# Kernel optimization log

Hardware: AMD Instinct MI355X
Metric: run time of the kernel (lower is better)

## Reference

```python
import jax, jax.numpy as jnp
import numpy as np

B, MAXT, MAXU, A = 16, 200, 101, 512
BLANK = 0


def setup_inputs() -> dict:
    key = jax.random.key(0)
    k1, k2, k3, k4 = jax.random.split(key, 4)
    logits = jax.random.normal(k1, (B, MAXT, MAXU, A), dtype=jnp.float32)
    log_probs = jax.nn.log_softmax(logits, axis=-1)  # transducer expects log-softmaxed acts
    labels = jax.random.randint(k2, (B, MAXU - 1), 1, A, dtype=jnp.int32)  # non-blank targets
    T = jax.random.randint(k3, (B,), MAXT // 2, MAXT + 1, dtype=jnp.int32)  # frames per utt
    U = jax.random.randint(k4, (B,), (MAXU - 1) // 2, MAXU, dtype=jnp.int32)  # labels per utt, <= MAXU-1
    return {"log_probs": log_probs, "labels": labels, "T": T, "U": U}


def _alpha_lattice(blk, emit):
    """RNN-T forward variables.
    blk, emit: [B, T, U] log-probs of blank / correct label at each lattice cell.
    Recurrence: alpha[t,u] = logaddexp(alpha[t-1,u]+blk[t-1,u], alpha[t,u-1]+emit[t,u-1]).
    Within a time step the u-recursion is solved in closed form with a
    log-cumsum-exp (associative_scan of logaddexp), so the only sequential
    loop is the scan over t.
    """
    Bb, Tm, Um = blk.shape

    def prefix_emit(emit_t):  # c[u] = sum_{k<u} emit_t[k]
        return jnp.concatenate(
            [jnp.zeros((Bb, 1), emit_t.dtype), jnp.cumsum(emit_t[:, :-1], axis=1)], axis=1)

    alpha0 = prefix_emit(emit[:, 0])  # alpha[0,u] = sum of first u emits, alpha[0,0]=0

    def step(alpha_prev, inputs):
        blk_tm1, emit_t = inputs            # [B, U] each
        a = alpha_prev + blk_tm1            # no-emit entry point per u
        c = prefix_emit(emit_t)
        # alpha[t,u] = c[u] + LSE_{u'<=u}(a[u'] - c[u'])
        alpha_t = c + jax.lax.associative_scan(jnp.logaddexp, a - c, axis=1)
        return alpha_t, alpha_t

    xs = (jnp.moveaxis(blk[:, :-1], 1, 0), jnp.moveaxis(emit[:, 1:], 1, 0))
    _, rest = jax.lax.scan(step, alpha0, xs)          # [T-1, B, U]
    alpha = jnp.concatenate([alpha0[None], rest], axis=0)  # [T, B, U]
    return jnp.moveaxis(alpha, 0, 1)                  # [B, T, U]


def reference(log_probs, labels, T, U):
    Bb, Tm, Um, _ = log_probs.shape
    blk = log_probs[..., BLANK]                       # [B, T, U]
    lab = jnp.concatenate([labels, jnp.zeros((Bb, 1), labels.dtype)], axis=1)  # pad to [B, U]
    idx = jnp.broadcast_to(lab[:, None, :, None], (Bb, Tm, Um, 1))
    emit = jnp.take_along_axis(log_probs, idx, axis=3)[..., 0]  # log P(label_u | t, u)
    alpha = _alpha_lattice(blk, emit)
    bidx = jnp.arange(Bb)
    # log_p = alpha[T-1, U] + blank emission at terminal cell (== beta[0,0])
    log_p = alpha[bidx, T - 1, U] + blk[bidx, T - 1, U]
    return jnp.mean(-log_p)  # reduction='mean'; -(lpa+lpb)/2 == -log_p exactly
```

## Files before the change

kernel.cpp:

```cpp
#include <hip/hip_runtime.h>
#include <math.h>


#define BATCH 16
#define TMAX  200
#define UMAX  101
#define VOC   512
#define NTHR  128
#define DEPTH 4

__device__ __forceinline__ float lse2(float a, float b) {
    float m = fmaxf(a, b);
    float r = m + __logf(__expf(a - m) + __expf(b - m));
    return (m == -INFINITY) ? -INFINITY : r;
}

__global__ __launch_bounds__(NTHR) void rnnt_fwd_kernel(
    const float* __restrict__ lp,
    const int*   __restrict__ labels,
    const int*   __restrict__ Tarr,
    const int*   __restrict__ Uarr,
    float*       __restrict__ out)
{
    const int b = blockIdx.x;
    const int u = threadIdx.x;

    __shared__ float As[2][NTHR];

    const int Tb = Tarr[b];
    const int Ub = Uarr[b];
    const float* lpb = lp + (size_t)b * TMAX * UMAX * VOC;

    int labm1 = 0;
    if (u >= 1 && u <= UMAX - 1) labm1 = labels[b * (UMAX - 1) + (u - 1)];

    const float NEG = -INFINITY;
    float A = (u == 0) ? 0.0f : NEG;
    As[0][u] = A;
    __syncthreads();

    const int dmax = Tb - 1 + Ub;
    const bool loader = (u <= Ub);

    float pb[DEPTH], pe[DEPTH];
    auto ld = [&](int d, float& vb, float& ve) {
        int t   = d - u;
        int tb_ = min(max(t - 1, 0), TMAX - 1);
        int te_ = min(max(t,     0), TMAX - 1);
        int ue_ = max(u - 1, 0);
        if (loader) {
            vb = lpb[((size_t)tb_ * UMAX + u)   * VOC];
            ve = lpb[((size_t)te_ * UMAX + ue_) * VOC + labm1];
        } else { vb = 0.0f; ve = 0.0f; }
    };

#pragma unroll
    for (int j = 0; j < DEPTH; ++j) {
        int d = 1 + j;
        ld(d <= dmax ? d : dmax, pb[j], pe[j]);
    }

    for (int dbase = 1; dbase <= dmax; dbase += DEPTH) {
        float cb[DEPTH], ce[DEPTH];
#pragma unroll
        for (int j = 0; j < DEPTH; ++j) { cb[j] = pb[j]; ce[j] = pe[j]; }
#pragma unroll
        for (int j = 0; j < DEPTH; ++j) {
            int dn = dbase + DEPTH + j;
            ld(dn <= dmax ? dn : dmax, pb[j], pe[j]);
        }
#pragma unroll
        for (int j = 0; j < DEPTH; ++j) {
            const int d = dbase + j;
            if (d > dmax) break;
            const int t = d - u;
            const bool active = (u <= Ub) && (u <= d) && (t <= Tb - 1);
            const float left  = As[(d - 1) & 1][(u == 0) ? 0 : (u - 1)];
            const float top   = (active && t >= 1) ? (A    + cb[j]) : NEG;
            const float lft   = (active && u >= 1) ? (left + ce[j]) : NEG;
            const float An    = active ? lse2(top, lft) : NEG;
            As[d & 1][u] = An;
            A = An;
            __syncthreads();
        }
    }

    if (u == Ub) {
        const float blk_fin = lpb[((size_t)(Tb - 1) * UMAX + Ub) * VOC];
        atomicAdd(out, -(A + blk_fin) * (1.0f / BATCH));
    }
}

extern "C" void kernel_launch(void* const* d_in, const int* in_sizes, int n_in,
                              void* d_out, int out_size, void* d_ws, size_t ws_size,
                              hipStream_t stream) {
    const float* lp     = (const float*)d_in[0];
    const int*   labels = (const int*)d_in[1];
    const int*   Tarr   = (const int*)d_in[2];
    const int*   Uarr   = (const int*)d_in[3];
    float* out = (float*)d_out;

    hipMemsetAsync(out, 0, sizeof(float), stream);
    rnnt_fwd_kernel<<<BATCH, NTHR, 0, stream>>>(lp, labels, Tarr, Uarr, out);
}
```

Baseline: 896.7 us.

## Split into parallel diagonal gather plus single-wavefront shuffle-based sweep

Adds a massively parallel gather kernel that pre-extracts blank and emit log-probs into a diagonal-major, contiguous workspace. The sequential sweep then runs on one 64-lane wavefront per batch, with each lane holding two u cells and exchanging neighbours through __shfl_up, so the per-diagonal __syncthreads and shared-memory traffic go away. The sweep's loads become coalesced float2 reads, prefetched DEPTH=8 diagonals ahead. The cost is an extra kernel launch and an intermediate workspace write and read.

```diff
diff --git a/kernel.cpp b/kernel.cpp
--- a/kernel.cpp
+++ b/kernel.cpp
@@ -6,88 +6,91 @@
 #define TMAX  200
 #define UMAX  101
 #define VOC   512
-#define NTHR  128
-#define DEPTH 4
+#define NDIAG (TMAX + UMAX - 1)
+#define PITCH 128
+#define DEPTH 8
+#define NEGINF (-INFINITY)
 
 __device__ __forceinline__ float lse2(float a, float b) {
     float m = fmaxf(a, b);
     float r = m + __logf(__expf(a - m) + __expf(b - m));
-    return (m == -INFINITY) ? -INFINITY : r;
+    return (m == NEGINF) ? NEGINF : r;
 }
 
-__global__ __launch_bounds__(NTHR) void rnnt_fwd_kernel(
+__global__ __launch_bounds__(PITCH) void gather_kernel(
+    const float* __restrict__ lp, const int* __restrict__ labels,
+    float* __restrict__ Dblk, float* __restrict__ Demit)
+{
+    const int d = blockIdx.x;
+    const int b = blockIdx.y;
+    const int u = threadIdx.x;
+    const size_t row = ((size_t)b * NDIAG + d) * PITCH + u;
+
+    const int tt = d - u - 1;
+    float vb = NEGINF;
+    if (u < UMAX && tt >= 0 && tt < TMAX)
+        vb = lp[(((size_t)b * TMAX + tt) * UMAX + u) * VOC];
+
+    const int te = d - u;
+    float ve = NEGINF;
+    if (u >= 1 && u < UMAX && te >= 0 && te < TMAX) {
+        const int lab = labels[b * (UMAX - 1) + (u - 1)];
+        ve = lp[(((size_t)b * TMAX + te) * UMAX + (u - 1)) * VOC + lab];
+    }
+    Dblk[row]  = vb;
+    Demit[row] = ve;
+}
+
+__global__ __launch_bounds__(64) void sweep_kernel(
+    const float* __restrict__ Dblk, const float* __restrict__ Demit,
     const float* __restrict__ lp,
-    const int*   __restrict__ labels,
-    const int*   __restrict__ Tarr,
-    const int*   __restrict__ Uarr,
-    float*       __restrict__ out)
+    const int* __restrict__ Tarr, const int* __restrict__ Uarr,
+    float* __restrict__ out)
 {
-    const int b = blockIdx.x;
-    const int u = threadIdx.x;
+    const int b    = blockIdx.x;
+    const int lane = threadIdx.x;
+    const int Tb   = Tarr[b];
+    const int Ub   = Uarr[b];
+    const int dmax = Tb - 1 + Ub;
 
-    __shared__ float As[2][NTHR];
+    const float2* rb = (const float2*)(Dblk  + (size_t)b * NDIAG * PITCH);
+    const float2* re = (const float2*)(Demit + (size_t)b * NDIAG * PITCH);
 
-    const int Tb = Tarr[b];
-    const int Ub = Uarr[b];
-    const float* lpb = lp + (size_t)b * TMAX * UMAX * VOC;
+    float A0 = (lane == 0) ? 0.0f : NEGINF;
+    float A1 = NEGINF;
 
-    int labm1 = 0;
-    if (u >= 1 && u <= UMAX - 1) labm1 = labels[b * (UMAX - 1) + (u - 1)];
-
-    const float NEG = -INFINITY;
-    float A = (u == 0) ? 0.0f : NEG;
-    As[0][u] = A;
-    __syncthreads();
-
-    const int dmax = Tb - 1 + Ub;
-    const bool loader = (u <= Ub);
-
-    float pb[DEPTH], pe[DEPTH];
-    auto ld = [&](int d, float& vb, float& ve) {
-        int t   = d - u;
-        int tb_ = min(max(t - 1, 0), TMAX - 1);
-        int te_ = min(max(t,     0), TMAX - 1);
-        int ue_ = max(u - 1, 0);
-        if (loader) {
-            vb = lpb[((size_t)tb_ * UMAX + u)   * VOC];
-            ve = lpb[((size_t)te_ * UMAX + ue_) * VOC + labm1];
-        } else { vb = 0.0f; ve = 0.0f; }
-    };
-
+    float2 qb[DEPTH], qe[DEPTH];
 #pragma unroll
     for (int j = 0; j < DEPTH; ++j) {
-        int d = 1 + j;
-        ld(d <= dmax ? d : dmax, pb[j], pe[j]);
+        int d = min(1 + j, dmax);
+        qb[j] = rb[d * 64 + lane];
+        qe[j] = re[d * 64 + lane];
     }
 
     for (int dbase = 1; dbase <= dmax; dbase += DEPTH) {
-        float cb[DEPTH], ce[DEPTH];
+        float2 cb[DEPTH], ce[DEPTH];
 #pragma unroll
-        for (int j = 0; j < DEPTH; ++j) { cb[j] = pb[j]; ce[j] = pe[j]; }
+        for (int j = 0; j < DEPTH; ++j) { cb[j] = qb[j]; ce[j] = qe[j]; }
 #pragma unroll
         for (int j = 0; j < DEPTH; ++j) {
-            int dn = dbase + DEPTH + j;
-            ld(dn <= dmax ? dn : dmax, pb[j], pe[j]);
+            int dn = min(dbase + DEPTH + j, dmax);
+            qb[j] = rb[dn * 64 + lane];
+            qe[j] = re[dn * 64 + lane];
         }
 #pragma unroll
         for (int j = 0; j < DEPTH; ++j) {
-            const int d = dbase + j;
-            if (d > dmax) break;
-            const int t = d - u;
-            const bool active = (u <= Ub) && (u <= d) && (t <= Tb - 1);
-            const float left  = As[(d - 1) & 1][(u == 0) ? 0 : (u - 1)];
-            const float top   = (active && t >= 1) ? (A    + cb[j]) : NEG;
-            const float lft   = (active && u >= 1) ? (left + ce[j]) : NEG;
-            const float An    = active ? lse2(top, lft) : NEG;
-            As[d & 1][u] = An;
-            A = An;
-            __syncthreads();
+            if (dbase + j > dmax) break;
+            float Aup = __shfl_up(A1, 1);
+            float n0 = lse2(A0 + cb[j].x, Aup + ce[j].x);
+            float n1 = lse2(A1 + cb[j].y, A0  + ce[j].y);
+            A0 = n0; A1 = n1;
         }
     }
 
-    if (u == Ub) {
-        const float blk_fin = lpb[((size_t)(Tb - 1) * UMAX + Ub) * VOC];
-        atomicAdd(out, -(A + blk_fin) * (1.0f / BATCH));
+    if (lane == (Ub >> 1)) {
+        float Af   = (Ub & 1) ? A1 : A0;
+        float blkf = lp[(((size_t)b * TMAX + (Tb - 1)) * UMAX + Ub) * VOC];
+        atomicAdd(out, -(Af + blkf) * (1.0f / BATCH));
     }
 }
 
@@ -100,6 +103,12 @@
     const int*   Uarr   = (const int*)d_in[3];
     float* out = (float*)d_out;
 
+    float* Dblk  = (float*)d_ws;
+    float* Demit = Dblk + (size_t)BATCH * NDIAG * PITCH;
+
     hipMemsetAsync(out, 0, sizeof(float), stream);
-    rnnt_fwd_kernel<<<BATCH, NTHR, 0, stream>>>(lp, labels, Tarr, Uarr, out);
+
+    dim3 g1(NDIAG, BATCH);
+    gather_kernel<<<g1, PITCH, 0, stream>>>(lp, labels, Dblk, Demit);
+    sweep_kernel<<<BATCH, 64, 0, stream>>>(Dblk, Demit, lp, Tarr, Uarr, out);
 }
```

New measurement: 762.6 us. 15.0% less time.
